# Kernel optimization log

Measured on AMD Instinct MI355X. Metric: run time of the kernel, lower is better.

Reference implementation:

```python
import jax, jax.numpy as jnp
import numpy as np

N_DST = 25000
E = 400000
DN = 128   # dim_node
DE = 128   # dim_edge
DT = 128   # dim_time
DO = 128   # dim_out
H = 2      # num_head


def setup_inputs() -> dict:
    key = jax.random.key(0)
    ks = jax.random.split(key, 10)
    sc = 0.05
    node_h = jax.random.normal(ks[0], (N_DST + E, DN), jnp.float32)
    edge_f = jax.random.normal(ks[1], (E, DE), jnp.float32)
    dt = jax.random.uniform(ks[2], (E,), jnp.float32) * 100.0
    dst_idx = jax.random.randint(ks[3], (E,), 0, N_DST)
    # TimeEncode: Linear(1, dim_time) with w initialized to 1/10**linspace(0,9)
    time_w = jnp.asarray(1.0 / 10 ** np.linspace(0, 9, DT, dtype=np.float32))
    time_b = jnp.zeros((DT,), jnp.float32)
    Wq = jax.random.normal(ks[4], (DO, DN + DT), jnp.float32) * sc
    bq = jnp.zeros((DO,), jnp.float32)
    Wk = jax.random.normal(ks[5], (DO, DN + DE + DT), jnp.float32) * sc
    bk = jnp.zeros((DO,), jnp.float32)
    Wv = jax.random.normal(ks[6], (DO, DN + DE + DT), jnp.float32) * sc
    bv = jnp.zeros((DO,), jnp.float32)
    Wout = jax.random.normal(ks[7], (DO, DN + DO), jnp.float32) * sc
    bout = jnp.zeros((DO,), jnp.float32)
    gamma = jnp.ones((DO,), jnp.float32)
    beta = jnp.zeros((DO,), jnp.float32)
    return dict(node_h=node_h, edge_f=edge_f, dt=dt, dst_idx=dst_idx,
                time_w=time_w, time_b=time_b, Wq=Wq, bq=bq, Wk=Wk, bk=bk,
                Wv=Wv, bv=bv, Wout=Wout, bout=bout, gamma=gamma, beta=beta)


def reference(node_h, edge_f, dt, dst_idx, time_w, time_b,
              Wq, bq, Wk, bk, Wv, bv, Wout, bout, gamma, beta):
    num_dst = node_h.shape[0] - edge_f.shape[0]
    num_edges = edge_f.shape[0]
    tgt = node_h[:num_dst]            # [N, DN] target node embeddings
    src = node_h[num_dst:]            # [E, DN] per-edge source embeddings

    # TimeEncode: cos(w * dt + b)
    time_feats = jnp.cos(dt[:, None] * time_w[None, :] + time_b)          # [E, DT]
    zero_time = jnp.broadcast_to(jnp.cos(time_b), (num_dst, time_b.shape[0]))

    Qn = jnp.concatenate([tgt, zero_time], axis=1) @ Wq.T + bq            # [N, DO]
    kv_in = jnp.concatenate([src, edge_f, time_feats], axis=1)            # [E, DN+DE+DT]
    K = kv_in @ Wk.T + bk                                                 # [E, DO]
    V = kv_in @ Wv.T + bv                                                 # [E, DO]
    Q = Qn[dst_idx]                                                       # gather per edge

    d_head = Q.shape[1] // H
    Qh = Q.reshape(num_edges, H, d_head)
    Kh = K.reshape(num_edges, H, d_head)
    Vh = V.reshape(num_edges, H, d_head)

    score = jnp.sum(Qh * Kh, axis=2)                                      # [E, H]
    score = jnp.where(score >= 0, score, 0.2 * score)                     # LeakyReLU(0.2)

    # edge_softmax: segmented softmax over incoming edges of each dst node
    m = jax.ops.segment_max(score, dst_idx, num_segments=num_dst)
    m = jnp.where(jnp.isfinite(m), m, 0.0)                                # empty segments
    e = jnp.exp(score - m[dst_idx])
    s = jax.ops.segment_sum(e, dst_idx, num_segments=num_dst)
    att = e / s[dst_idx]                                                  # [E, H]

    Vw = (Vh * att[:, :, None]).reshape(num_edges, -1)                    # [E, DO]
    h = jax.ops.segment_sum(Vw, dst_idx, num_segments=num_dst)            # scatter-sum

    rst = jnp.concatenate([h, tgt], axis=1) @ Wout.T + bout               # [N, DO]
    rst = jax.nn.relu(rst)
    mu = jnp.mean(rst, axis=-1, keepdims=True)
    var = jnp.var(rst, axis=-1, keepdims=True)
    return (rst - mu) / jnp.sqrt(var + 1e-5) * gamma + beta
```

## Files before the change

kernel.cpp:

```cpp
#include <hip/hip_runtime.h>

#define N_DST 25000
#define E_NUM 400000

typedef __bf16 bf16x8 __attribute__((ext_vector_type(8)));
typedef __bf16 bf16x4 __attribute__((ext_vector_type(4)));
typedef __bf16 bf16x2 __attribute__((ext_vector_type(2)));
typedef float  f32x4  __attribute__((ext_vector_type(4)));

__device__ __forceinline__ float fast_cos(float x) {
  float r = x * 0.15915494309189535f;
  r = r - floorf(r);
  return __builtin_amdgcn_cosf(r);
}

__global__ __launch_bounds__(128) void cq_kernel(const float* __restrict__ Wq,
    const float* __restrict__ bq, const float* __restrict__ tb, float* __restrict__ cq) {
  int o = threadIdx.x;
  float s = bq[o];
  for (int j = 0; j < 128; ++j) s += cosf(tb[j]) * Wq[o * 256 + 128 + j];
  cq[o] = s;
}

__global__ __launch_bounds__(256) void pack_kernel(const float* __restrict__ W0,
    const float* __restrict__ W1, int srcStride, int N, int total, __bf16* __restrict__ Bp) {
  int idx = blockIdx.x * 256 + threadIdx.x;
  if (idx >= total) return;
  int g = idx / N, n = idx - g * N;
  const float* src = (W1 && n >= 128) ? (W1 + (size_t)(n - 128) * srcStride)
                                      : (W0 + (size_t)n * srcStride);
  const float4* s4 = reinterpret_cast<const float4*>(src + g * 8);
  float4 lo = s4[0], hi = s4[1];
  bf16x8 b;
  b[0] = (__bf16)lo.x; b[1] = (__bf16)lo.y; b[2] = (__bf16)lo.z; b[3] = (__bf16)lo.w;
  b[4] = (__bf16)hi.x; b[5] = (__bf16)hi.y; b[6] = (__bf16)hi.z; b[7] = (__bf16)hi.w;
  reinterpret_cast<bf16x8*>(Bp)[idx] = b;
}

__global__ __launch_bounds__(256) void count_kernel(const int* __restrict__ dsti, int* __restrict__ counts) {
  int e = blockIdx.x * 256 + threadIdx.x;
  if (e < E_NUM) atomicAdd(&counts[dsti[e]], 1);
}

__global__ __launch_bounds__(1024) void scan_kernel(const int* __restrict__ counts,
    int* __restrict__ offs, int* __restrict__ cursor) {
  __shared__ int wpart[16];
  int tid = threadIdx.x, lane = tid & 63, wid = tid >> 6;
  int carry = 0;
  for (int base = 0; base < N_DST; base += 1024) {
    int idx = base + tid;
    int x = (idx < N_DST) ? counts[idx] : 0;
    int incl = x;
#pragma unroll
    for (int o = 1; o < 64; o <<= 1) {
      int y = __shfl_up(incl, o);
      if (lane >= o) incl += y;
    }
    if (lane == 63) wpart[wid] = incl;
    __syncthreads();
    if (wid == 0) {
      int v = (lane < 16) ? wpart[lane] : 0;
      int s = v;
#pragma unroll
      for (int o = 1; o < 16; o <<= 1) {
        int y = __shfl_up(s, o);
        if (lane >= o) s += y;
      }
      if (lane < 16) wpart[lane] = s;
    }
    __syncthreads();
    int woff = (wid > 0) ? wpart[wid - 1] : 0;
    int tot = wpart[15];
    if (idx < N_DST) {
      int v = carry + woff + incl - x;
      offs[idx] = v;
      cursor[idx] = v;
    }
    carry += tot;
    __syncthreads();
  }
  if (tid == 0) offs[N_DST] = carry;
}

__global__ __launch_bounds__(256) void fill_kernel(const int* __restrict__ dsti,
    int* __restrict__ cursor, int* __restrict__ elist, int* __restrict__ dsts) {
  int e = blockIdx.x * 256 + threadIdx.x;
  if (e < E_NUM) {
    int d = dsti[e];
    int p = atomicAdd(&cursor[d], 1);
    elist[p] = e;
    dsts[p] = d;
  }
}

template<int MODE>
__global__ __launch_bounds__(256, 3) void gemm_kernel(
    const float* __restrict__ A0, const float* __restrict__ A1,
    const float* __restrict__ dtp, const float* __restrict__ tw, const float* __restrict__ tb,
    const __bf16* __restrict__ Bp,
    const float* __restrict__ bias0, const float* __restrict__ bias1,
    const int* __restrict__ elist, const int* __restrict__ dsts,
    const float* __restrict__ Qn,
    float* __restrict__ outF, __bf16* __restrict__ Vout, float* __restrict__ score)
{
  constexpr int KD = (MODE == 0) ? 128 : ((MODE == 1) ? 384 : 256);
  constexpr int NC = (MODE == 1) ? 256 : 128;
  constexpr int KB = KD * 2;
  constexpr int NFRAG = NC / 64;
  constexpr int NK = KD / 32;
  __shared__ __align__(16) char Atile[64 * KB];
  __shared__ int Elds[64];
  __shared__ int Dlds[64];
  __shared__ float dts[64];
  __shared__ float twl[128];
  __shared__ float tbl[128];

  const int tid = threadIdx.x;
  const int e0 = blockIdx.x * 64;
  const int nv = (MODE == 1) ? 64 : min(64, N_DST - e0);

  if constexpr (MODE == 1) {
    if (tid < 64) {
      int e = elist[e0 + tid];
      Elds[tid] = e;
      Dlds[tid] = dsts[e0 + tid];
      dts[tid] = dtp[e];
    } else if (tid < 192) {
      int j = tid - 64;
      twl[j] = tw[j];
      tbl[j] = tb[j];
    }
    __syncthreads();
    float4 sv[8], ev[8];
#pragma unroll
    for (int i = 0; i < 8; ++i) {
      int c = tid + i * 256;
      int r = c >> 5, c4 = (c & 31) << 2;
      int eidx = Elds[r];
      sv[i] = *reinterpret_cast<const float4*>(A0 + ((size_t)N_DST + eidx) * 128 + c4);
      ev[i] = *reinterpret_cast<const float4*>(A1 + (size_t)eidx * 128 + c4);
    }
    {
      int r = tid >> 2;
      int j0 = (tid & 3) << 5;
      float d = dts[r];
      char* rowb = Atile + r * KB;
      int swz = (r & 7) << 4;
      const float2* tw2 = reinterpret_cast<const float2*>(twl);
      const float2* tb2 = reinterpret_cast<const float2*>(tbl);
#pragma unroll
      for (int i = 0; i < 16; ++i) {
        int j = j0 + i * 2;
        float2 wv = tw2[j >> 1], bv = tb2[j >> 1];
        bf16x2 p;
        p[0] = (__bf16)fast_cos(d * wv.x + bv.x);
        p[1] = (__bf16)fast_cos(d * wv.y + bv.y);
        *reinterpret_cast<bf16x2*>(rowb + ((512 + j * 2) ^ swz)) = p;
      }
    }
#pragma unroll
    for (int i = 0; i < 8; ++i) {
      int c = tid + i * 256;
      int r = c >> 5, c4 = (c & 31) << 2;
      bf16x4 b0, b1;
      b0[0] = (__bf16)sv[i].x; b0[1] = (__bf16)sv[i].y; b0[2] = (__bf16)sv[i].z; b0[3] = (__bf16)sv[i].w;
      b1[0] = (__bf16)ev[i].x; b1[1] = (__bf16)ev[i].y; b1[2] = (__bf16)ev[i].z; b1[3] = (__bf16)ev[i].w;
      *reinterpret_cast<bf16x4*>(Atile + r * KB + ((c4 * 2) ^ ((r & 7) << 4))) = b0;
      *reinterpret_cast<bf16x4*>(Atile + r * KB + ((256 + c4 * 2) ^ ((r & 7) << 4))) = b1;
    }
    __syncthreads();
  } else {
#pragma unroll
    for (int i = 0; i < 8; ++i) {
      int c = tid + i * 256;
      int r = c >> 5, c4 = (c & 31) << 2;
      float4 v0 = make_float4(0.f, 0.f, 0.f, 0.f);
      float4 v1 = make_float4(0.f, 0.f, 0.f, 0.f);
      if (r < nv) {
        v0 = *reinterpret_cast<const float4*>(A0 + (size_t)(e0 + r) * 128 + c4);
        if constexpr (MODE == 2)
          v1 = *reinterpret_cast<const float4*>(A1 + (size_t)(e0 + r) * 128 + c4);
      }
      bf16x4 b0;
      b0[0] = (__bf16)v0.x; b0[1] = (__bf16)v0.y; b0[2] = (__bf16)v0.z; b0[3] = (__bf16)v0.w;
      *reinterpret_cast<bf16x4*>(Atile + r * KB + ((c4 * 2) ^ ((r & 7) << 4))) = b0;
      if constexpr (MODE == 2) {
        bf16x4 b1;
        b1[0] = (__bf16)v1.x; b1[1] = (__bf16)v1.y; b1[2] = (__bf16)v1.z; b1[3] = (__bf16)v1.w;
        *reinterpret_cast<bf16x4*>(Atile + r * KB + ((256 + c4 * 2) ^ ((r & 7) << 4))) = b1;
      }
    }
    __syncthreads();
  }

  const int lane = tid & 63;
  const int w = tid >> 6;
  const int nbase = w * (NC / 4);
  const int lrow = lane & 15;
  const int lk = lane >> 4;
  const int aswz = (lrow & 7) << 4;

  f32x4 acc[4][NFRAG];
#pragma unroll
  for (int mf = 0; mf < 4; ++mf)
#pragma unroll
    for (int nf = 0; nf < NFRAG; ++nf)
      acc[mf][nf] = (f32x4){0.f, 0.f, 0.f, 0.f};

  const bf16x8* Bb = reinterpret_cast<const bf16x8*>(Bp) + (size_t)lk * NC + nbase + lrow;
  bf16x8 bq[3][NFRAG];
  bf16x8 aq[2][4];
  auto loadB = [&](int ks) {
#pragma unroll
    for (int nf = 0; nf < NFRAG; ++nf)
      bq[ks % 3][nf] = Bb[(size_t)ks * 4 * NC + nf * 16];
  };
  auto loadA = [&](int ks) {
#pragma unroll
    for (int mf = 0; mf < 4; ++mf)
      aq[ks % 2][mf] = *reinterpret_cast<const bf16x8*>(
          Atile + (mf * 16 + lrow) * KB + (((ks * 32 + lk * 8) * 2) ^ aswz));
  };
  loadB(0);
  if (NK > 1) loadB(1);
  loadA(0);
#pragma unroll
  for (int ks = 0; ks < NK; ++ks) {
    if (ks + 2 < NK) loadB(ks + 2);
    if (ks + 1 < NK) loadA(ks + 1);
#pragma unroll
    for (int nf = 0; nf < NFRAG; ++nf)
#pragma unroll
      for (int mf = 0; mf < 4; ++mf)
        acc[mf][nf] = __builtin_amdgcn_mfma_f32_16x16x32_bf16(aq[ks % 2][mf], bq[ks % 3][nf],
                                                              acc[mf][nf], 0, 0, 0);
  }

  if constexpr (MODE == 0) {
#pragma unroll
    for (int nf = 0; nf < NFRAG; ++nf) {
      int col = nbase + nf * 16 + lrow;
      float bb = bias0[col];
#pragma unroll
      for (int mf = 0; mf < 4; ++mf) {
#pragma unroll
        for (int r = 0; r < 4; ++r) {
          int row = mf * 16 + lk * 4 + r;
          if (row < nv)
            outF[(size_t)(e0 + row) * 128 + col] = acc[mf][nf][r] + bb;
        }
      }
    }
  } else if constexpr (MODE == 2) {
    const float* gammaP = dtp;
    const float* betaP = tw;
    float vals[2][4][4];
#pragma unroll
    for (int nf = 0; nf < 2; ++nf) {
      float bb = bias0[nbase + nf * 16 + lrow];
#pragma unroll
      for (int mf = 0; mf < 4; ++mf)
#pragma unroll
        for (int r = 0; r < 4; ++r)
          vals[nf][mf][r] = fmaxf(acc[mf][nf][r] + bb, 0.f);
    }
    __syncthreads();
    float* sums = reinterpret_cast<float*>(Atile);
    float* sqs  = reinterpret_cast<float*>(Atile) + 256;
    float* stats = reinterpret_cast<float*>(Atile) + 512;
#pragma unroll
    for (int mf = 0; mf < 4; ++mf) {
#pragma unroll
      for (int r = 0; r < 4; ++r) {
        float s1 = vals[0][mf][r] + vals[1][mf][r];
        float s2 = vals[0][mf][r] * vals[0][mf][r] + vals[1][mf][r] * vals[1][mf][r];
#pragma unroll
        for (int o = 1; o < 16; o <<= 1) {
          s1 += __shfl_xor(s1, o);
          s2 += __shfl_xor(s2, o);
        }
        if (lrow == 0) {
          int row = mf * 16 + lk * 4 + r;
          sums[w * 64 + row] = s1;
          sqs[w * 64 + row] = s2;
        }
      }
    }
    __syncthreads();
    if (tid < 64) {
      float s = sums[tid] + sums[64 + tid] + sums[128 + tid] + sums[192 + tid];
      float q = sqs[tid] + sqs[64 + tid] + sqs[128 + tid] + sqs[192 + tid];
      float mean = s * (1.f / 128.f);
      float var = q * (1.f / 128.f) - mean * mean;
      stats[tid * 2] = mean;
      stats[tid * 2 + 1] = rsqrtf(var + 1e-5f);
    }
    __syncthreads();
#pragma unroll
    for (int nf = 0; nf < 2; ++nf) {
      int col = nbase + nf * 16 + lrow;
      float g = gammaP[col], b = betaP[col];
#pragma unroll
      for (int mf = 0; mf < 4; ++mf) {
#pragma unroll
        for (int r = 0; r < 4; ++r) {
          int row = mf * 16 + lk * 4 + r;
          if (row < nv) {
            float mean = stats[row * 2], rs = stats[row * 2 + 1];
            outF[(size_t)(e0 + row) * 128 + col] = (vals[nf][mf][r] - mean) * rs * g + b;
          }
        }
      }
    }
  } else {
    __syncthreads();
    if (w >= 2) {
#pragma unroll
      for (int nf = 0; nf < 4; ++nf) {
        int vcol = (nbase - 128) + nf * 16 + lrow;
        float bb = bias1[vcol];
#pragma unroll
        for (int mf = 0; mf < 4; ++mf) {
#pragma unroll
          for (int r = 0; r < 4; ++r) {
            int row = mf * 16 + lk * 4 + r;
            *reinterpret_cast<__bf16*>(Atile + row * 256 + ((vcol * 2) ^ ((row & 7) << 4))) =
                (__bf16)(acc[mf][nf][r] + bb);
          }
        }
      }
    } else {
      float bkv[4];
#pragma unroll
      for (int nf = 0; nf < 4; ++nf) bkv[nf] = bias0[w * 64 + nf * 16 + lrow];
#pragma unroll
      for (int mf = 0; mf < 4; ++mf) {
#pragma unroll
        for (int r = 0; r < 4; ++r) {
          int row = mf * 16 + lk * 4 + r;
          const float* qrow = Qn + ((size_t)Dlds[row] << 7) + w * 64;
          float s = 0.f;
#pragma unroll
          for (int nf = 0; nf < 4; ++nf)
            s += (acc[mf][nf][r] + bkv[nf]) * qrow[nf * 16 + lrow];
          s += __shfl_xor(s, 1);
          s += __shfl_xor(s, 2);
          s += __shfl_xor(s, 4);
          s += __shfl_xor(s, 8);
          if (lrow == 0) {
            s = (s >= 0.f) ? s : 0.2f * s;
            score[((size_t)(e0 + row) << 1) + w] = s;
          }
        }
      }
    }
    __syncthreads();
#pragma unroll
    for (int i = 0; i < 4; ++i) {
      int c = tid + i * 256;
      int r = c >> 4, cb = (c & 15) << 4;
      bf16x8 v = *reinterpret_cast<const bf16x8*>(Atile + r * 256 + (cb ^ ((r & 7) << 4)));
      *reinterpret_cast<bf16x8*>(Vout + (((size_t)(e0 + r)) << 7) + (c & 15) * 8) = v;
    }
  }
}

__global__ __launch_bounds__(256) void agg_kernel(const int* __restrict__ offs,
    const float* __restrict__ score, const __bf16* __restrict__ V, float* __restrict__ h) {
  int d = blockIdx.x * 4 + (threadIdx.x >> 6);
  if (d >= N_DST) return;
  int lane = threadIdx.x & 63;
  int beg = offs[d], end = offs[d + 1];
  int n = end - beg;
  float m0 = -3.0e38f, m1 = -3.0e38f;
  for (int i = lane; i < n; i += 64) {
    float2 sc = *reinterpret_cast<const float2*>(score + 2 * (size_t)(beg + i));
    m0 = fmaxf(m0, sc.x); m1 = fmaxf(m1, sc.y);
  }
#pragma unroll
  for (int o = 32; o; o >>= 1) {
    m0 = fmaxf(m0, __shfl_xor(m0, o));
    m1 = fmaxf(m1, __shfl_xor(m1, o));
  }
  float s0 = 0.f, s1 = 0.f;
  for (int i = lane; i < n; i += 64) {
    float2 sc = *reinterpret_cast<const float2*>(score + 2 * (size_t)(beg + i));
    s0 += __expf(sc.x - m0); s1 += __expf(sc.y - m1);
  }
#pragma unroll
  for (int o = 32; o; o >>= 1) {
    s0 += __shfl_xor(s0, o);
    s1 += __shfl_xor(s1, o);
  }
  float inv0 = (n > 0) ? 1.f / s0 : 0.f;
  float inv1 = (n > 0) ? 1.f / s1 : 0.f;
  int q = lane >> 4, j = lane & 15;
  int hsel = j >> 3;
  float acc[8];
#pragma unroll
  for (int k2 = 0; k2 < 8; ++k2) acc[k2] = 0.f;
  for (int i0 = 0; i0 < n; i0 += 4) {
    int i = i0 + q;
    if (i < n) {
      size_t p = beg + i;
      float2 sc = *reinterpret_cast<const float2*>(score + 2 * p);
      float wgt = hsel ? __expf(sc.y - m1) * inv1 : __expf(sc.x - m0) * inv0;
      bf16x8 v = *reinterpret_cast<const bf16x8*>(V + (p << 7) + j * 8);
#pragma unroll
      for (int k2 = 0; k2 < 8; ++k2) acc[k2] += wgt * (float)v[k2];
    }
  }
#pragma unroll
  for (int k2 = 0; k2 < 8; ++k2) {
    acc[k2] += __shfl_xor(acc[k2], 16);
    acc[k2] += __shfl_xor(acc[k2], 32);
  }
  if (q == 0) {
    float4 lo = make_float4(acc[0], acc[1], acc[2], acc[3]);
    float4 hi = make_float4(acc[4], acc[5], acc[6], acc[7]);
    float* dst = h + ((size_t)d << 7) + j * 8;
    *reinterpret_cast<float4*>(dst) = lo;
    *reinterpret_cast<float4*>(dst + 4) = hi;
  }
}

extern "C" void kernel_launch(void* const* d_in, const int* in_sizes, int n_in,
                              void* d_out, int out_size, void* d_ws, size_t ws_size,
                              hipStream_t stream) {
  (void)in_sizes; (void)n_in; (void)out_size; (void)ws_size;
  const float* node_h = (const float*)d_in[0];
  const float* edge_f = (const float*)d_in[1];
  const float* dtp    = (const float*)d_in[2];
  const int*   dsti   = (const int*)d_in[3];
  const float* tw     = (const float*)d_in[4];
  const float* tb     = (const float*)d_in[5];
  const float* Wq     = (const float*)d_in[6];
  const float* bq     = (const float*)d_in[7];
  const float* Wk     = (const float*)d_in[8];
  const float* bk     = (const float*)d_in[9];
  const float* Wv     = (const float*)d_in[10];
  const float* bv     = (const float*)d_in[11];
  const float* Wout   = (const float*)d_in[12];
  const float* bout   = (const float*)d_in[13];
  const float* gamma  = (const float*)d_in[14];
  const float* beta   = (const float*)d_in[15];
  float* outp = (float*)d_out;

  size_t off = 0;
  auto take = [&](size_t nbytes) -> void* {
    void* r = (char*)d_ws + off;
    off += (nbytes + 255) & ~(size_t)255;
    return r;
  };
  __bf16* Bp_kv  = (__bf16*)take((size_t)48 * 256 * 8 * 2);
  __bf16* Bp_q   = (__bf16*)take((size_t)16 * 128 * 8 * 2);
  __bf16* Bp_out = (__bf16*)take((size_t)32 * 128 * 8 * 2);
  float*  cq     = (float*)take(128 * 4);
  float*  Qn     = (float*)take((size_t)N_DST * 128 * 4);
  __bf16* Vbuf   = (__bf16*)take((size_t)E_NUM * 128 * 2);
  float*  score  = (float*)take((size_t)E_NUM * 2 * 4);
  int*    counts = (int*)take((size_t)N_DST * 4);
  int*    offs   = (int*)take((size_t)(N_DST + 1) * 4);
  int*    cursor = (int*)take((size_t)N_DST * 4);
  int*    elist  = (int*)take((size_t)E_NUM * 4);
  int*    dsts   = (int*)take((size_t)E_NUM * 4);
  float*  hbuf   = (float*)take((size_t)N_DST * 128 * 4);

  hipMemsetAsync(counts, 0, (size_t)N_DST * 4, stream);

  cq_kernel<<<1, 128, 0, stream>>>(Wq, bq, tb, cq);
  pack_kernel<<<(48 * 256 + 255) / 256, 256, 0, stream>>>(Wk, Wv, 384, 256, 48 * 256, Bp_kv);
  pack_kernel<<<(16 * 128 + 255) / 256, 256, 0, stream>>>(Wq, nullptr, 256, 128, 16 * 128, Bp_q);
  pack_kernel<<<(32 * 128 + 255) / 256, 256, 0, stream>>>(Wout, nullptr, 256, 128, 32 * 128, Bp_out);

  count_kernel<<<(E_NUM + 255) / 256, 256, 0, stream>>>(dsti, counts);
  scan_kernel<<<1, 1024, 0, stream>>>(counts, offs, cursor);
  fill_kernel<<<(E_NUM + 255) / 256, 256, 0, stream>>>(dsti, cursor, elist, dsts);

  gemm_kernel<0><<<(N_DST + 63) / 64, 256, 0, stream>>>(node_h, nullptr, nullptr, nullptr, nullptr,
      Bp_q, cq, nullptr, nullptr, nullptr, nullptr, Qn, nullptr, nullptr);
  gemm_kernel<1><<<E_NUM / 64, 256, 0, stream>>>(node_h, edge_f, dtp, tw, tb,
      Bp_kv, bk, bv, elist, dsts, Qn, nullptr, Vbuf, score);

  agg_kernel<<<(N_DST + 3) / 4, 256, 0, stream>>>(offs, score, Vbuf, hbuf);

  gemm_kernel<2><<<(N_DST + 63) / 64, 256, 0, stream>>>(hbuf, node_h, gamma, beta, nullptr,
      Bp_out, bout, nullptr, nullptr, nullptr, nullptr, outp, nullptr, nullptr);
}
```

Measured before the change: 368.9 us.

## Stream A tiles through double-buffered LDS and pre-swizzle B into fragment order

The GEMM kernels now stage A in 128-wide K chunks through two LDS buffers, so the global gather of the next chunk overlaps the MFMA work on the current one. The time-encoding cos chunk is computed last. Shared memory per block drops from 48KB to 32KB, which lets launch bounds rise to 4 blocks per SM. Weights are packed into a per-wave, per-lane fragment order so B loads are contiguous, and the cq, pack and count kernels are merged into one prep kernel to cut launches. The cost is more barriers per tile and B fragments loaded without deep prefetch, which may expose latency.

Measured after the change: 341.0 us. 7.6% less time.

```diff
diff --git a/kernel.cpp b/kernel.cpp
--- a/kernel.cpp
+++ b/kernel.cpp
@@ -14,31 +14,48 @@
   return __builtin_amdgcn_cosf(r);
 }
 
-__global__ __launch_bounds__(128) void cq_kernel(const float* __restrict__ Wq,
-    const float* __restrict__ bq, const float* __restrict__ tb, float* __restrict__ cq) {
-  int o = threadIdx.x;
-  float s = bq[o];
-  for (int j = 0; j < 128; ++j) s += cosf(tb[j]) * Wq[o * 256 + 128 + j];
-  cq[o] = s;
-}
-
-__global__ __launch_bounds__(256) void pack_kernel(const float* __restrict__ W0,
-    const float* __restrict__ W1, int srcStride, int N, int total, __bf16* __restrict__ Bp) {
-  int idx = blockIdx.x * 256 + threadIdx.x;
-  if (idx >= total) return;
-  int g = idx / N, n = idx - g * N;
-  const float* src = (W1 && n >= 128) ? (W1 + (size_t)(n - 128) * srcStride)
-                                      : (W0 + (size_t)n * srcStride);
+__device__ __forceinline__ void pack_frag(const float* __restrict__ W0,
+    const float* __restrict__ W1, int stride, int NC, int idx, __bf16* __restrict__ out) {
+  int lane = idx & 63, fid = idx >> 6;
+  int nfw = NC >> 6;
+  int perks = nfw << 2;
+  int ks = fid / perks, rem = fid - ks * perks;
+  int w = rem / nfw, nf = rem - w * nfw;
+  int n = w * (NC >> 2) + nf * 16 + (lane & 15);
+  int g = (ks << 2) + (lane >> 4);
+  const float* src = (W1 && n >= 128) ? (W1 + (size_t)(n - 128) * stride)
+                                      : (W0 + (size_t)n * stride);
   const float4* s4 = reinterpret_cast<const float4*>(src + g * 8);
   float4 lo = s4[0], hi = s4[1];
   bf16x8 b;
-  b[0] = (__bf16)lo.x; b[1] = (__bf16)lo.y; b[2] = (__bf16)lo.z; b[3] = (__bf16)lo.w;
-  b[4] = (__bf16)hi.x; b[5] = (__bf16)hi.y; b[6] = (__bf16)hi.z; b[7] = (__bf16)hi.w;
-  reinterpret_cast<bf16x8*>(Bp)[idx] = b;
-}
-
-__global__ __launch_bounds__(256) void count_kernel(const int* __restrict__ dsti, int* __restrict__ counts) {
-  int e = blockIdx.x * 256 + threadIdx.x;
+  b[0]=(__bf16)lo.x; b[1]=(__bf16)lo.y; b[2]=(__bf16)lo.z; b[3]=(__bf16)lo.w;
+  b[4]=(__bf16)hi.x; b[5]=(__bf16)hi.y; b[6]=(__bf16)hi.z; b[7]=(__bf16)hi.w;
+  reinterpret_cast<bf16x8*>(out)[idx] = b;
+}
+
+__global__ __launch_bounds__(256) void prep_kernel(
+    const float* __restrict__ Wq, const float* __restrict__ bq, const float* __restrict__ tb,
+    const float* __restrict__ Wk, const float* __restrict__ Wv, const float* __restrict__ Wout,
+    const int* __restrict__ dsti,
+    float* __restrict__ cq, __bf16* __restrict__ Bq_kv, __bf16* __restrict__ Bq_q,
+    __bf16* __restrict__ Bq_out, int* __restrict__ counts) {
+  int b = blockIdx.x, tid = threadIdx.x;
+  if (b == 0) {
+    if (tid < 128) {
+      float s = bq[tid];
+      for (int j = 0; j < 128; ++j) s += cosf(tb[j]) * Wq[tid * 256 + 128 + j];
+      cq[tid] = s;
+    }
+    return;
+  }
+  b -= 1;
+  if (b < 48) { pack_frag(Wk, Wv, 384, 256, b * 256 + tid, Bq_kv); return; }
+  b -= 48;
+  if (b < 8)  { pack_frag(Wq, nullptr, 256, 128, b * 256 + tid, Bq_q); return; }
+  b -= 8;
+  if (b < 16) { pack_frag(Wout, nullptr, 256, 128, b * 256 + tid, Bq_out); return; }
+  b -= 16;
+  int e = b * 256 + tid;
   if (e < E_NUM) atomicAdd(&counts[dsti[e]], 1);
 }
 
@@ -94,21 +111,18 @@
 }
 
 template<int MODE>
-__global__ __launch_bounds__(256, 3) void gemm_kernel(
+__global__ __launch_bounds__(256, 4) void gemm_kernel(
     const float* __restrict__ A0, const float* __restrict__ A1,
     const float* __restrict__ dtp, const float* __restrict__ tw, const float* __restrict__ tb,
-    const __bf16* __restrict__ Bp,
+    const __bf16* __restrict__ Bq,
     const float* __restrict__ bias0, const float* __restrict__ bias1,
     const int* __restrict__ elist, const int* __restrict__ dsts,
     const float* __restrict__ Qn,
     float* __restrict__ outF, __bf16* __restrict__ Vout, float* __restrict__ score)
 {
-  constexpr int KD = (MODE == 0) ? 128 : ((MODE == 1) ? 384 : 256);
   constexpr int NC = (MODE == 1) ? 256 : 128;
-  constexpr int KB = KD * 2;
-  constexpr int NFRAG = NC / 64;
-  constexpr int NK = KD / 32;
-  __shared__ __align__(16) char Atile[64 * KB];
+  constexpr int NFRAGW = NC / 64;
+  __shared__ __align__(16) char Abuf[2][64 * 256];
   __shared__ int Elds[64];
   __shared__ int Dlds[64];
   __shared__ float dts[64];
@@ -118,6 +132,84 @@
   const int tid = threadIdx.x;
   const int e0 = blockIdx.x * 64;
   const int nv = (MODE == 1) ? 64 : min(64, N_DST - e0);
+  const int srow = tid >> 5;
+  const int sc4 = (tid & 31) << 2;
+
+  const int lane = tid & 63;
+  const int w = tid >> 6;
+  const int nbase = w * (NC / 4);
+  const int lrow = lane & 15;
+  const int lk = lane >> 4;
+  const int aswz = (lrow & 7) << 4;
+  const bf16x8* __restrict__ Bw =
+      reinterpret_cast<const bf16x8*>(Bq) + (size_t)(w * NFRAGW) * 64 + lane;
+
+  f32x4 acc[4][NFRAGW];
+#pragma unroll
+  for (int mf = 0; mf < 4; ++mf)
+#pragma unroll
+    for (int nf = 0; nf < NFRAGW; ++nf)
+      acc[mf][nf] = (f32x4){0.f, 0.f, 0.f, 0.f};
+
+  auto issueA = [&](int t, float4 (&v)[8]) {
+    if constexpr (MODE == 1) {
+      const float* base = (t == 0) ? (A0 + (size_t)N_DST * 128) : A1;
+#pragma unroll
+      for (int i = 0; i < 8; ++i)
+        v[i] = *reinterpret_cast<const float4*>(base + (size_t)Elds[srow + i * 8] * 128 + sc4);
+    } else {
+      const float* base = (t == 0) ? A0 : A1;
+#pragma unroll
+      for (int i = 0; i < 8; ++i) {
+        int r = srow + i * 8;
+        v[i] = (r < nv) ? *reinterpret_cast<const float4*>(base + (size_t)(e0 + r) * 128 + sc4)
+                        : make_float4(0.f, 0.f, 0.f, 0.f);
+      }
+    }
+  };
+  auto writeA = [&](char* buf, float4 (&v)[8]) {
+#pragma unroll
+    for (int i = 0; i < 8; ++i) {
+      int r = srow + i * 8;
+      bf16x4 b;
+      b[0]=(__bf16)v[i].x; b[1]=(__bf16)v[i].y; b[2]=(__bf16)v[i].z; b[3]=(__bf16)v[i].w;
+      *reinterpret_cast<bf16x4*>(buf + r * 256 + ((sc4 * 2) ^ ((r & 7) << 4))) = b;
+    }
+  };
+  auto cosW = [&](char* buf) {
+    int r = tid >> 2;
+    int j0 = (tid & 3) << 5;
+    float d = dts[r];
+    char* rowb = buf + r * 256;
+    int swz = (r & 7) << 4;
+#pragma unroll
+    for (int i = 0; i < 16; ++i) {
+      int j = j0 + i * 2;
+      bf16x2 p;
+      p[0] = (__bf16)fast_cos(d * twl[j] + tbl[j]);
+      p[1] = (__bf16)fast_cos(d * twl[j + 1] + tbl[j + 1]);
+      *reinterpret_cast<bf16x2*>(rowb + ((j * 2) ^ swz)) = p;
+    }
+  };
+  auto ktile = [&](const char* buf, int t) {
+#pragma unroll
+    for (int ks = 0; ks < 4; ++ks) {
+      bf16x8 b[NFRAGW];
+#pragma unroll
+      for (int nf = 0; nf < NFRAGW; ++nf)
+        b[nf] = Bw[((size_t)(t * 4 + ks) * 4 * NFRAGW + nf) * 64];
+      bf16x8 a[4];
+#pragma unroll
+      for (int mf = 0; mf < 4; ++mf)
+        a[mf] = *reinterpret_cast<const bf16x8*>(
+            buf + (mf * 16 + lrow) * 256 + (((ks * 32 + lk * 8) * 2) ^ aswz));
+#pragma unroll
+      for (int nf = 0; nf < NFRAGW; ++nf)
+#pragma unroll
+        for (int mf = 0; mf < 4; ++mf)
+          acc[mf][nf] = __builtin_amdgcn_mfma_f32_16x16x32_bf16(a[mf], b[nf], acc[mf][nf], 0, 0, 0);
+    }
+  };
 
   if constexpr (MODE == 1) {
     if (tid < 64) {
@@ -131,192 +223,22 @@
       tbl[j] = tb[j];
     }
     __syncthreads();
-    float4 sv[8], ev[8];
-#pragma unroll
-    for (int i = 0; i < 8; ++i) {
-      int c = tid + i * 256;
-      int r = c >> 5, c4 = (c & 31) << 2;
-      int eidx = Elds[r];
-      sv[i] = *reinterpret_cast<const float4*>(A0 + ((size_t)N_DST + eidx) * 128 + c4);
-      ev[i] = *reinterpret_cast<const float4*>(A1 + (size_t)eidx * 128 + c4);
-    }
-    {
-      int r = tid >> 2;
-      int j0 = (tid & 3) << 5;
-      float d = dts[r];
-      char* rowb = Atile + r * KB;
-      int swz = (r & 7) << 4;
-      const float2* tw2 = reinterpret_cast<const float2*>(twl);
-      const float2* tb2 = reinterpret_cast<const float2*>(tbl);
-#pragma unroll
-      for (int i = 0; i < 16; ++i) {
-        int j = j0 + i * 2;
-        float2 wv = tw2[j >> 1], bv = tb2[j >> 1];
-        bf16x2 p;
-        p[0] = (__bf16)fast_cos(d * wv.x + bv.x);
-        p[1] = (__bf16)fast_cos(d * wv.y + bv.y);
-        *reinterpret_cast<bf16x2*>(rowb + ((512 + j * 2) ^ swz)) = p;
-      }
-    }
-#pragma unroll
-    for (int i = 0; i < 8; ++i) {
-      int c = tid + i * 256;
-      int r = c >> 5, c4 = (c & 31) << 2;
-      bf16x4 b0, b1;
-      b0[0] = (__bf16)sv[i].x; b0[1] = (__bf16)sv[i].y; b0[2] = (__bf16)sv[i].z; b0[3] = (__bf16)sv[i].w;
-      b1[0] = (__bf16)ev[i].x; b1[1] = (__bf16)ev[i].y; b1[2] = (__bf16)ev[i].z; b1[3] = (__bf16)ev[i].w;
-      *reinterpret_cast<bf16x4*>(Atile + r * KB + ((c4 * 2) ^ ((r & 7) << 4))) = b0;
-      *reinterpret_cast<bf16x4*>(Atile + r * KB + ((256 + c4 * 2) ^ ((r & 7) << 4))) = b1;
-    }
-    __syncthreads();
-  } else {
-#pragma unroll
-    for (int i = 0; i < 8; ++i) {
-      int c = tid + i * 256;
-      int r = c >> 5, c4 = (c & 31) << 2;
-      float4 v0 = make_float4(0.f, 0.f, 0.f, 0.f);
-      float4 v1 = make_float4(0.f, 0.f, 0.f, 0.f);
-      if (r < nv) {
-        v0 = *reinterpret_cast<const float4*>(A0 + (size_t)(e0 + r) * 128 + c4);
-        if constexpr (MODE == 2)
-          v1 = *reinterpret_cast<const float4*>(A1 + (size_t)(e0 + r) * 128 + c4);
-      }
-      bf16x4 b0;
-      b0[0] = (__bf16)v0.x; b0[1] = (__bf16)v0.y; b0[2] = (__bf16)v0.z; b0[3] = (__bf16)v0.w;
-      *reinterpret_cast<bf16x4*>(Atile + r * KB + ((c4 * 2) ^ ((r & 7) << 4))) = b0;
-      if constexpr (MODE == 2) {
-        bf16x4 b1;
-        b1[0] = (__bf16)v1.x; b1[1] = (__bf16)v1.y; b1[2] = (__bf16)v1.z; b1[3] = (__bf16)v1.w;
-        *reinterpret_cast<bf16x4*>(Atile + r * KB + ((256 + c4 * 2) ^ ((r & 7) << 4))) = b1;
-      }
-    }
-    __syncthreads();
-  }
-
-  const int lane = tid & 63;
-  const int w = tid >> 6;
-  const int nbase = w * (NC / 4);
-  const int lrow = lane & 15;
-  const int lk = lane >> 4;
-  const int aswz = (lrow & 7) << 4;
-
-  f32x4 acc[4][NFRAG];
-#pragma unroll
-  for (int mf = 0; mf < 4; ++mf)
-#pragma unroll
-    for (int nf = 0; nf < NFRAG; ++nf)
-      acc[mf][nf] = (f32x4){0.f, 0.f, 0.f, 0.f};
-
-  const bf16x8* Bb = reinterpret_cast<const bf16x8*>(Bp) + (size_t)lk * NC + nbase + lrow;
-  bf16x8 bq[3][NFRAG];
-  bf16x8 aq[2][4];
-  auto loadB = [&](int ks) {
-#pragma unroll
-    for (int nf = 0; nf < NFRAG; ++nf)
-      bq[ks % 3][nf] = Bb[(size_t)ks * 4 * NC + nf * 16];
-  };
-  auto loadA = [&](int ks) {
-#pragma unroll
-    for (int mf = 0; mf < 4; ++mf)
-      aq[ks % 2][mf] = *reinterpret_cast<const bf16x8*>(
-          Atile + (mf * 16 + lrow) * KB + (((ks * 32 + lk * 8) * 2) ^ aswz));
-  };
-  loadB(0);
-  if (NK > 1) loadB(1);
-  loadA(0);
-#pragma unroll
-  for (int ks = 0; ks < NK; ++ks) {
-    if (ks + 2 < NK) loadB(ks + 2);
-    if (ks + 1 < NK) loadA(ks + 1);
-#pragma unroll
-    for (int nf = 0; nf < NFRAG; ++nf)
-#pragma unroll
-      for (int mf = 0; mf < 4; ++mf)
-        acc[mf][nf] = __builtin_amdgcn_mfma_f32_16x16x32_bf16(aq[ks % 2][mf], bq[ks % 3][nf],
-                                                              acc[mf][nf], 0, 0, 0);
-  }
-
-  if constexpr (MODE == 0) {
-#pragma unroll
-    for (int nf = 0; nf < NFRAG; ++nf) {
-      int col = nbase + nf * 16 + lrow;
-      float bb = bias0[col];
-#pragma unroll
-      for (int mf = 0; mf < 4; ++mf) {
-#pragma unroll
-        for (int r = 0; r < 4; ++r) {
-          int row = mf * 16 + lk * 4 + r;
-          if (row < nv)
-            outF[(size_t)(e0 + row) * 128 + col] = acc[mf][nf][r] + bb;
-        }
-      }
-    }
-  } else if constexpr (MODE == 2) {
-    const float* gammaP = dtp;
-    const float* betaP = tw;
-    float vals[2][4][4];
-#pragma unroll
-    for (int nf = 0; nf < 2; ++nf) {
-      float bb = bias0[nbase + nf * 16 + lrow];
-#pragma unroll
-      for (int mf = 0; mf < 4; ++mf)
-#pragma unroll
-        for (int r = 0; r < 4; ++r)
-          vals[nf][mf][r] = fmaxf(acc[mf][nf][r] + bb, 0.f);
-    }
-    __syncthreads();
-    float* sums = reinterpret_cast<float*>(Atile);
-    float* sqs  = reinterpret_cast<float*>(Atile) + 256;
-    float* stats = reinterpret_cast<float*>(Atile) + 512;
-#pragma unroll
-    for (int mf = 0; mf < 4; ++mf) {
-#pragma unroll
-      for (int r = 0; r < 4; ++r) {
-        float s1 = vals[0][mf][r] + vals[1][mf][r];
-        float s2 = vals[0][mf][r] * vals[0][mf][r] + vals[1][mf][r] * vals[1][mf][r];
-#pragma unroll
-        for (int o = 1; o < 16; o <<= 1) {
-          s1 += __shfl_xor(s1, o);
-          s2 += __shfl_xor(s2, o);
-        }
-        if (lrow == 0) {
-          int row = mf * 16 + lk * 4 + r;
-          sums[w * 64 + row] = s1;
-          sqs[w * 64 + row] = s2;
-        }
-      }
-    }
-    __syncthreads();
-    if (tid < 64) {
-      float s = sums[tid] + sums[64 + tid] + sums[128 + tid] + sums[192 + tid];
-      float q = sqs[tid] + sqs[64 + tid] + sqs[128 + tid] + sqs[192 + tid];
-      float mean = s * (1.f / 128.f);
-      float var = q * (1.f / 128.f) - mean * mean;
-      stats[tid * 2] = mean;
-      stats[tid * 2 + 1] = rsqrtf(var + 1e-5f);
-    }
-    __syncthreads();
-#pragma unroll
-    for (int nf = 0; nf < 2; ++nf) {
-      int col = nbase + nf * 16 + lrow;
-      float g = gammaP[col], b = betaP[col];
-#pragma unroll
-      for (int mf = 0; mf < 4; ++mf) {
-#pragma unroll
-        for (int r = 0; r < 4; ++r) {
-          int row = mf * 16 + lk * 4 + r;
-          if (row < nv) {
-            float mean = stats[row * 2], rs = stats[row * 2 + 1];
-            outF[(size_t)(e0 + row) * 128 + col] = (vals[nf][mf][r] - mean) * rs * g + b;
-          }
-        }
-      }
-    }
-  } else {
+    float4 v[8];
+    issueA(0, v);
+    writeA(Abuf[0], v);
+    __syncthreads();
+    issueA(1, v);
+    ktile(Abuf[0], 0);
+    writeA(Abuf[1], v);
+    __syncthreads();
+    ktile(Abuf[1], 1);
+    cosW(Abuf[0]);
+    __syncthreads();
+    ktile(Abuf[0], 2);
     __syncthreads();
     if (w >= 2) {
 #pragma unroll
-      for (int nf = 0; nf < 4; ++nf) {
+      for (int nf = 0; nf < NFRAGW; ++nf) {
         int vcol = (nbase - 128) + nf * 16 + lrow;
         float bb = bias1[vcol];
 #pragma unroll
@@ -324,15 +246,15 @@
 #pragma unroll
           for (int r = 0; r < 4; ++r) {
             int row = mf * 16 + lk * 4 + r;
-            *reinterpret_cast<__bf16*>(Atile + row * 256 + ((vcol * 2) ^ ((row & 7) << 4))) =
+            *reinterpret_cast<__bf16*>(Abuf[0] + row * 256 + ((vcol * 2) ^ ((row & 7) << 4))) =
                 (__bf16)(acc[mf][nf][r] + bb);
           }
         }
       }
     } else {
-      float bkv[4];
-#pragma unroll
-      for (int nf = 0; nf < 4; ++nf) bkv[nf] = bias0[w * 64 + nf * 16 + lrow];
+      float bkv[NFRAGW];
+#pragma unroll
+      for (int nf = 0; nf < NFRAGW; ++nf) bkv[nf] = bias0[nbase + nf * 16 + lrow];
 #pragma unroll
       for (int mf = 0; mf < 4; ++mf) {
 #pragma unroll
@@ -341,7 +263,7 @@
           const float* qrow = Qn + ((size_t)Dlds[row] << 7) + w * 64;
           float s = 0.f;
 #pragma unroll
-          for (int nf = 0; nf < 4; ++nf)
+          for (int nf = 0; nf < NFRAGW; ++nf)
             s += (acc[mf][nf][r] + bkv[nf]) * qrow[nf * 16 + lrow];
           s += __shfl_xor(s, 1);
           s += __shfl_xor(s, 2);
@@ -359,8 +281,98 @@
     for (int i = 0; i < 4; ++i) {
       int c = tid + i * 256;
       int r = c >> 4, cb = (c & 15) << 4;
-      bf16x8 v = *reinterpret_cast<const bf16x8*>(Atile + r * 256 + (cb ^ ((r & 7) << 4)));
-      *reinterpret_cast<bf16x8*>(Vout + (((size_t)(e0 + r)) << 7) + (c & 15) * 8) = v;
+      bf16x8 vv = *reinterpret_cast<const bf16x8*>(Abuf[0] + r * 256 + (cb ^ ((r & 7) << 4)));
+      *reinterpret_cast<bf16x8*>(Vout + (((size_t)(e0 + r)) << 7) + (c & 15) * 8) = vv;
+    }
+  } else if constexpr (MODE == 0) {
+    float4 v[8];
+    issueA(0, v);
+    writeA(Abuf[0], v);
+    __syncthreads();
+    ktile(Abuf[0], 0);
+#pragma unroll
+    for (int nf = 0; nf < NFRAGW; ++nf) {
+      int col = nbase + nf * 16 + lrow;
+      float bb = bias0[col];
+#pragma unroll
+      for (int mf = 0; mf < 4; ++mf) {
+#pragma unroll
+        for (int r = 0; r < 4; ++r) {
+          int row = mf * 16 + lk * 4 + r;
+          if (row < nv)
+            outF[(size_t)(e0 + row) * 128 + col] = acc[mf][nf][r] + bb;
+        }
+      }
+    }
+  } else {
+    float4 v[8];
+    issueA(0, v);
+    writeA(Abuf[0], v);
+    __syncthreads();
+    issueA(1, v);
+    ktile(Abuf[0], 0);
+    writeA(Abuf[1], v);
+    __syncthreads();
+    ktile(Abuf[1], 1);
+    const float* gammaP = dtp;
+    const float* betaP = tw;
+    float vals[NFRAGW][4][4];
+#pragma unroll
+    for (int nf = 0; nf < NFRAGW; ++nf) {
+      float bb = bias0[nbase + nf * 16 + lrow];
+#pragma unroll
+      for (int mf = 0; mf < 4; ++mf)
+#pragma unroll
+        for (int r = 0; r < 4; ++r)
+          vals[nf][mf][r] = fmaxf(acc[mf][nf][r] + bb, 0.f);
+    }
+    __syncthreads();
+    float* sums = reinterpret_cast<float*>(Abuf[0]);
+    float* sqs  = reinterpret_cast<float*>(Abuf[0]) + 256;
+    float* stats = reinterpret_cast<float*>(Abuf[0]) + 512;
+#pragma unroll
+    for (int mf = 0; mf < 4; ++mf) {
+#pragma unroll
+      for (int r = 0; r < 4; ++r) {
+        float s1 = vals[0][mf][r] + vals[1][mf][r];
+        float s2 = vals[0][mf][r] * vals[0][mf][r] + vals[1][mf][r] * vals[1][mf][r];
+#pragma unroll
+        for (int o = 1; o < 16; o <<= 1) {
+          s1 += __shfl_xor(s1, o);
+          s2 += __shfl_xor(s2, o);
+        }
+        if (lrow == 0) {
+          int row = mf * 16 + lk * 4 + r;
+          sums[w * 64 + row] = s1;
+          sqs[w * 64 + row] = s2;
+        }
+      }
+    }
+    __syncthreads();
+    if (tid < 64) {
+      float s = sums[tid] + sums[64 + tid] + sums[128 + tid] + sums[192 + tid];
+      float q = sqs[tid] + sqs[64 + tid] + sqs[128 + tid] + sqs[192 + tid];
+      float mean = s * (1.f / 128.f);
+      float var = q * (1.f / 128.f) - mean * mean;
+      stats[tid * 2] = mean;
+      stats[tid * 2 + 1] = rsqrtf(var + 1e-5f);
+    }
+    __syncthreads();
+#pragma unroll
+    for (int nf = 0; nf < NFRAGW; ++nf) {
+      int col = nbase + nf * 16 + lrow;
+      float g = gammaP[col], bC = betaP[col];
+#pragma unroll
+      for (int mf = 0; mf < 4; ++mf) {
+#pragma unroll
+        for (int r = 0; r < 4; ++r) {
+          int row = mf * 16 + lk * 4 + r;
+          if (row < nv) {
+            float mean = stats[row * 2], rs = stats[row * 2 + 1];
+            outF[(size_t)(e0 + row) * 128 + col] = (vals[nf][mf][r] - mean) * rs * g + bC;
+          }
+        }
+      }
     }
   }
 }
@@ -452,9 +464,9 @@
     off += (nbytes + 255) & ~(size_t)255;
     return r;
   };
-  __bf16* Bp_kv  = (__bf16*)take((size_t)48 * 256 * 8 * 2);
-  __bf16* Bp_q   = (__bf16*)take((size_t)16 * 128 * 8 * 2);
-  __bf16* Bp_out = (__bf16*)take((size_t)32 * 128 * 8 * 2);
+  __bf16* Bq_kv  = (__bf16*)take((size_t)12288 * 16);
+  __bf16* Bq_q   = (__bf16*)take((size_t)2048 * 16);
+  __bf16* Bq_out = (__bf16*)take((size_t)4096 * 16);
   float*  cq     = (float*)take(128 * 4);
   float*  Qn     = (float*)take((size_t)N_DST * 128 * 4);
   __bf16* Vbuf   = (__bf16*)take((size_t)E_NUM * 128 * 2);
@@ -468,22 +480,21 @@
 
   hipMemsetAsync(counts, 0, (size_t)N_DST * 4, stream);
 
-  cq_kernel<<<1, 128, 0, stream>>>(Wq, bq, tb, cq);
-  pack_kernel<<<(48 * 256 + 255) / 256, 256, 0, stream>>>(Wk, Wv, 384, 256, 48 * 256, Bp_kv);
-  pack_kernel<<<(16 * 128 + 255) / 256, 256, 0, stream>>>(Wq, nullptr, 256, 128, 16 * 128, Bp_q);
-  pack_kernel<<<(32 * 128 + 255) / 256, 256, 0, stream>>>(Wout, nullptr, 256, 128, 32 * 128, Bp_out);
-
-  count_kernel<<<(E_NUM + 255) / 256, 256, 0, stream>>>(dsti, counts);
+  const int count_blocks = (E_NUM + 255) / 256;
+  prep_kernel<<<1 + 48 + 8 + 16 + count_blocks, 256, 0, stream>>>(
+      Wq, bq, tb, Wk, Wv, Wout, dsti, cq, Bq_kv, Bq_q, Bq_out, counts);
+
+  gemm_kernel<0><<<(N_DST + 63) / 64, 256, 0, stream>>>(node_h, nullptr, nullptr, nullptr, nullptr,
+      Bq_q, cq, nullptr, nullptr, nullptr, nullptr, Qn, nullptr, nullptr);
+
   scan_kernel<<<1, 1024, 0, stream>>>(counts, offs, cursor);
-  fill_kernel<<<(E_NUM + 255) / 256, 256, 0, stream>>>(dsti, cursor, elist, dsts);
-
-  gemm_kernel<0><<<(N_DST + 63) / 64, 256, 0, stream>>>(node_h, nullptr, nullptr, nullptr, nullptr,
-      Bp_q, cq, nullptr, nullptr, nullptr, nullptr, Qn, nullptr, nullptr);
+  fill_kernel<<<count_blocks, 256, 0, stream>>>(dsti, cursor, elist, dsts);
+
   gemm_kernel<1><<<E_NUM / 64, 256, 0, stream>>>(node_h, edge_f, dtp, tw, tb,
-      Bp_kv, bk, bv, elist, dsts, Qn, nullptr, Vbuf, score);
+      Bq_kv, bk, bv, elist, dsts, Qn, nullptr, Vbuf, score);
 
   agg_kernel<<<(N_DST + 3) / 4, 256, 0, stream>>>(offs, score, Vbuf, hbuf);
 
   gemm_kernel<2><<<(N_DST + 63) / 64, 256, 0, stream>>>(hbuf, node_h, gamma, beta, nullptr,
-      Bp_out, bout, nullptr, nullptr, nullptr, nullptr, outp, nullptr, nullptr);
-}
+      Bq_out, bout, nullptr, nullptr, nullptr, nullptr, outp, nullptr, nullptr);
+}
```
